# Kernel tuning notes

Measured on AMD Instinct MI355X. Metric: run time of the kernel, lower is better.

## Reference

```python
import jax, jax.numpy as jnp
import numpy as np

L, B, H = 4096, 32, 512


def setup_inputs() -> dict:
    key = jax.random.key(0)
    k1, k2, k3, k4 = jax.random.split(key, 4)
    query = jax.random.normal(k1, (B, H), dtype=jnp.float32)
    key_val = jax.random.normal(k2, (L, B, H), dtype=jnp.float32)
    # torch Linear(2H, H, bias=False): weight is (H, 2H); we store transposed (2H, H)
    W = jax.random.normal(k3, (2 * H, H), dtype=jnp.float32) * (1.0 / np.sqrt(2 * H))
    v = jax.random.normal(k4, (H,), dtype=jnp.float32)
    return {"query": query, "key_val": key_val, "W": W, "v": v}


def reference(query, key_val, W, v):
    # concat([expand(query), key], -1) @ W == query @ W_q + key @ W_k
    Wq, Wk = W[:H], W[H:]                       # each (H, H)
    q_proj = query @ Wq                          # (B, H)
    k_proj = jnp.einsum('lbi,ih->lbh', key_val, Wk)  # (L, B, H)
    energy = jnp.tanh(q_proj[None, :, :] + k_proj)   # (L, B, H)
    scores = jnp.einsum('h,lbh->bl', v, energy)      # (B, L)
    return jax.nn.softmax(scores, axis=1)[:, None, :]  # (B, 1, L)
```

## Files before the change

kernel.cpp:

```cpp
#include <hip/hip_runtime.h>
#include <hip/hip_bf16.h>
#include <stdint.h>

#define L_DIM 4096
#define B_DIM 32
#define H_DIM 512
#define M_DIM (L_DIM * B_DIM)
#define K_DIM H_DIM

typedef _Float16 half8 __attribute__((ext_vector_type(8)));
typedef __fp16 fp16x2 __attribute__((ext_vector_type(2)));
typedef float floatx4 __attribute__((ext_vector_type(4)));

__device__ __forceinline__ float tanh_fast(float x) {
  float e = __builtin_amdgcn_exp2f(x * 2.88539008177793f);
  return 1.0f - 2.0f * __builtin_amdgcn_rcpf(e + 1.0f);
}

__device__ __forceinline__ uint2 pack4(const float4& f) {
  const fp16x2 p0 = __builtin_amdgcn_cvt_pkrtz(f.x, f.y);
  const fp16x2 p1 = __builtin_amdgcn_cvt_pkrtz(f.z, f.w);
  uint2 u;
  u.x = __builtin_bit_cast(unsigned, p0);
  u.y = __builtin_bit_cast(unsigned, p1);
  return u;
}

__global__ __launch_bounds__(128) void qproj_kernel(const float* __restrict__ query,
                                                    const float* __restrict__ W,
                                                    float* __restrict__ qp) {
  const int b = blockIdx.x;
  const int h = threadIdx.x * 4;
  const float* qrow = query + b * H_DIM;
  float4 acc = make_float4(0.f, 0.f, 0.f, 0.f);
#pragma unroll 8
  for (int i = 0; i < K_DIM; ++i) {
    const float qv = qrow[i];
    const float4 w4 = *(const float4*)(W + (size_t)i * H_DIM + h);
    acc.x += qv * w4.x; acc.y += qv * w4.y;
    acc.z += qv * w4.z; acc.w += qv * w4.w;
  }
  *(float4*)(qp + (size_t)b * H_DIM + h) = acc;
}

__global__ __launch_bounds__(256) void wconv_kernel(const float* __restrict__ W,
                                                    _Float16* __restrict__ W2) {
  const int t = blockIdx.x * 256 + threadIdx.x;
  const int l15 = t & 15;
  const int q = (t >> 4) & 3;
  const int nc = (t >> 6) & 31;
  const int kt = t >> 11;
  const int n = nc * 16 + l15;
  const int kbase = H_DIM + kt * 32 + q * 8;
  half8 h;
#pragma unroll
  for (int j = 0; j < 8; ++j)
    h[j] = (_Float16)W[(size_t)(kbase + j) * H_DIM + n];
  *(half8*)(W2 + (size_t)t * 8) = h;
}

__global__ __launch_bounds__(256, 2) void fused_gemm_kernel(
    const float* __restrict__ key, const _Float16* __restrict__ W2,
    const float* __restrict__ qp, const float* __restrict__ v,
    float* __restrict__ scores) {
  __shared__ __align__(16) _Float16 As[2][64 * 40];
  __shared__ float swave[256];

  const int tid = threadIdx.x;
  const int lane = tid & 63;
  const int w = tid >> 6;
  const int l15 = lane & 15;
  const int quad = lane >> 4;
  const int m0 = blockIdx.x * 64;

  const int ar = tid >> 3;
  const int aseg = tid & 7;
  const float* ag0 = key + (size_t)(m0 + ar) * K_DIM + aseg * 4;
  const float* ag1 = ag0 + (size_t)32 * K_DIM;
  const int adst0 = ar * 40 + aseg * 4;
  const int adst1 = (ar + 32) * 40 + aseg * 4;

  const half8* bptr = (const half8*)W2 + (size_t)(w * 8) * 64 + lane;

  int aoff[4];
#pragma unroll
  for (int fm = 0; fm < 4; ++fm) aoff[fm] = (fm * 16 + l15) * 40 + quad * 8;

  floatx4 acc[4][8];
#pragma unroll
  for (int fm = 0; fm < 4; ++fm)
#pragma unroll
    for (int fn = 0; fn < 8; ++fn) acc[fm][fn] = (floatx4)0.0f;

  float4 ra0 = *(const float4*)(ag0);
  float4 ra1 = *(const float4*)(ag1);
  half8 bn[8];
#pragma unroll
  for (int fn = 0; fn < 8; ++fn) bn[fn] = bptr[fn * 64];
  bptr += 32 * 64;
  *(uint2*)(As[0] + adst0) = pack4(ra0);
  *(uint2*)(As[0] + adst1) = pack4(ra1);
  ra0 = *(const float4*)(ag0 + 32);
  ra1 = *(const float4*)(ag1 + 32);
  __syncthreads();

  for (int kt = 0; kt < 16; ++kt) {
    half8 bc[8];
#pragma unroll
    for (int fn = 0; fn < 8; ++fn) bc[fn] = bn[fn];
    if (kt < 15) {
#pragma unroll
      for (int fn = 0; fn < 8; ++fn) bn[fn] = bptr[fn * 64];
      bptr += 32 * 64;
    }
    half8 av[4];
#pragma unroll
    for (int fm = 0; fm < 4; ++fm) av[fm] = *(const half8*)(As[kt & 1] + aoff[fm]);
    if (kt < 15) {
      _Float16* dst = As[(kt + 1) & 1];
      *(uint2*)(dst + adst0) = pack4(ra0);
      *(uint2*)(dst + adst1) = pack4(ra1);
      if (kt < 14) {
        ra0 = *(const float4*)(ag0 + (kt + 2) * 32);
        ra1 = *(const float4*)(ag1 + (kt + 2) * 32);
      }
    }
#pragma unroll
    for (int fm = 0; fm < 4; ++fm)
#pragma unroll
      for (int fn = 0; fn < 8; ++fn)
        acc[fm][fn] = __builtin_amdgcn_mfma_f32_16x16x32_f16(av[fm], bc[fn],
                                                             acc[fm][fn], 0, 0, 0);
    __syncthreads();
  }

  float vv[8];
#pragma unroll
  for (int fn = 0; fn < 8; ++fn) vv[fn] = v[w * 128 + fn * 16 + l15];

#pragma unroll
  for (int fm = 0; fm < 4; ++fm) {
#pragma unroll
    for (int r = 0; r < 4; ++r) {
      const int mrow = fm * 16 + quad * 4 + r;
      const float* qrow = qp + (size_t)(mrow & 31) * H_DIM;
      float rs = 0.f;
#pragma unroll
      for (int fn = 0; fn < 8; ++fn) {
        const int n = w * 128 + fn * 16 + l15;
        const float x = qrow[n] + acc[fm][fn][r];
        rs += vv[fn] * tanh_fast(x);
      }
      rs += __shfl_xor(rs, 1);
      rs += __shfl_xor(rs, 2);
      rs += __shfl_xor(rs, 4);
      rs += __shfl_xor(rs, 8);
      if (l15 == 0) swave[w * 64 + mrow] = rs;
    }
  }
  __syncthreads();
  if (tid < 64) {
    const float s = swave[tid] + swave[64 + tid] + swave[128 + tid] + swave[192 + tid];
    const int m = m0 + tid;
    scores[(size_t)(m & 31) * L_DIM + (m >> 5)] = s;
  }
}

__global__ __launch_bounds__(256) void softmax_kernel(const float* __restrict__ scores,
                                                      float* __restrict__ out) {
  const int b = blockIdx.x;
  const int t = threadIdx.x;
  __shared__ float red[256];
  const float* srow = scores + (size_t)b * L_DIM;
  float s[16];
#pragma unroll
  for (int i = 0; i < 16; ++i) s[i] = srow[t + i * 256];
  float mx = s[0];
#pragma unroll
  for (int i = 1; i < 16; ++i) mx = fmaxf(mx, s[i]);
  red[t] = mx;
  __syncthreads();
  for (int off = 128; off > 0; off >>= 1) {
    if (t < off) red[t] = fmaxf(red[t], red[t + off]);
    __syncthreads();
  }
  mx = red[0];
  __syncthreads();
  float sum = 0.f;
#pragma unroll
  for (int i = 0; i < 16; ++i) {
    s[i] = __builtin_amdgcn_exp2f((s[i] - mx) * 1.44269504f);
    sum += s[i];
  }
  red[t] = sum;
  __syncthreads();
  for (int off = 128; off > 0; off >>= 1) {
    if (t < off) red[t] += red[t + off];
    __syncthreads();
  }
  const float inv = 1.0f / red[0];
#pragma unroll
  for (int i = 0; i < 16; ++i) out[(size_t)b * L_DIM + t + i * 256] = s[i] * inv;
}

extern "C" void kernel_launch(void* const* d_in, const int* in_sizes, int n_in,
                              void* d_out, int out_size, void* d_ws, size_t ws_size,
                              hipStream_t stream) {
  const float* query = (const float*)d_in[0];
  const float* key   = (const float*)d_in[1];
  const float* W     = (const float*)d_in[2];
  const float* v     = (const float*)d_in[3];
  float* out = (float*)d_out;

  char* ws = (char*)d_ws;
  float* qp       = (float*)ws;
  float* scores   = (float*)(ws + 65536);
  _Float16* W2    = (_Float16*)(ws + 65536 + 524288);

  qproj_kernel<<<32, 128, 0, stream>>>(query, W, qp);
  wconv_kernel<<<128, 256, 0, stream>>>(W, W2);
  fused_gemm_kernel<<<M_DIM / 64, 256, 0, stream>>>(key, W2, qp, v, scores);
  softmax_kernel<<<B_DIM, 256, 0, stream>>>(scores, out);
}
```

Before: 446.8 us.

## Stage full A tile in swizzled LDS and drop per-k-step barriers

Loads the entire 64x512 key tile for a block into LDS as fp16 up front, using an XOR swizzle to avoid bank conflicts. The K loop then runs without any __syncthreads, prefetching the next A fragments from LDS into registers. This removes the per-iteration barriers and the double-buffer store traffic. In exchange LDS use grows to 64 KB per block, which can limit occupancy, and all global loads are issued before any compute, so load/compute overlap within a block is lost.

Result: slower. 485.7 us (+8.7%).

```diff
diff --git a/kernel.cpp b/kernel.cpp
--- a/kernel.cpp
+++ b/kernel.cpp
@@ -63,8 +63,7 @@
     const float* __restrict__ key, const _Float16* __restrict__ W2,
     const float* __restrict__ qp, const float* __restrict__ v,
     float* __restrict__ scores) {
-  __shared__ __align__(16) _Float16 As[2][64 * 40];
-  __shared__ float swave[256];
+  __shared__ __align__(16) _Float16 As[64 * 512];
 
   const int tid = threadIdx.x;
   const int lane = tid & 63;
@@ -73,18 +72,24 @@
   const int quad = lane >> 4;
   const int m0 = blockIdx.x * 64;
 
-  const int ar = tid >> 3;
-  const int aseg = tid & 7;
-  const float* ag0 = key + (size_t)(m0 + ar) * K_DIM + aseg * 4;
-  const float* ag1 = ag0 + (size_t)32 * K_DIM;
-  const int adst0 = ar * 40 + aseg * 4;
-  const int adst1 = (ar + 32) * 40 + aseg * 4;
+  {
+    const float* gsrc = key + (size_t)m0 * K_DIM;
+#pragma unroll
+    for (int i = 0; i < 32; ++i) {
+      const int c = i * 256 + tid;
+      const float4 f = *(const float4*)(gsrc + 4 * c);
+      const int row = c >> 7;
+      const int off = row * 1024 + ((((c & 127) >> 1) ^ (row & 7)) << 4) + (c & 1) * 8;
+      *(uint2*)((char*)As + off) = pack4(f);
+    }
+  }
 
   const half8* bptr = (const half8*)W2 + (size_t)(w * 8) * 64 + lane;
 
-  int aoff[4];
-#pragma unroll
-  for (int fm = 0; fm < 4; ++fm) aoff[fm] = (fm * 16 + l15) * 40 + quad * 8;
+  int abase[4];
+#pragma unroll
+  for (int fm = 0; fm < 4; ++fm) abase[fm] = (fm * 16 + l15) * 1024;
+  const int xorv = l15 & 7;
 
   floatx4 acc[4][8];
 #pragma unroll
@@ -92,38 +97,34 @@
 #pragma unroll
     for (int fn = 0; fn < 8; ++fn) acc[fm][fn] = (floatx4)0.0f;
 
-  float4 ra0 = *(const float4*)(ag0);
-  float4 ra1 = *(const float4*)(ag1);
   half8 bn[8];
 #pragma unroll
   for (int fn = 0; fn < 8; ++fn) bn[fn] = bptr[fn * 64];
   bptr += 32 * 64;
-  *(uint2*)(As[0] + adst0) = pack4(ra0);
-  *(uint2*)(As[0] + adst1) = pack4(ra1);
-  ra0 = *(const float4*)(ag0 + 32);
-  ra1 = *(const float4*)(ag1 + 32);
-  __syncthreads();
+
+  __syncthreads();
+
+  half8 av[4];
+  {
+    const int coff = ((0 * 4 + quad) ^ xorv) << 4;
+#pragma unroll
+    for (int fm = 0; fm < 4; ++fm)
+      av[fm] = *(const half8*)((const char*)As + abase[fm] + coff);
+  }
 
   for (int kt = 0; kt < 16; ++kt) {
     half8 bc[8];
 #pragma unroll
     for (int fn = 0; fn < 8; ++fn) bc[fn] = bn[fn];
+    half8 an[4];
     if (kt < 15) {
 #pragma unroll
       for (int fn = 0; fn < 8; ++fn) bn[fn] = bptr[fn * 64];
       bptr += 32 * 64;
-    }
-    half8 av[4];
-#pragma unroll
-    for (int fm = 0; fm < 4; ++fm) av[fm] = *(const half8*)(As[kt & 1] + aoff[fm]);
-    if (kt < 15) {
-      _Float16* dst = As[(kt + 1) & 1];
-      *(uint2*)(dst + adst0) = pack4(ra0);
-      *(uint2*)(dst + adst1) = pack4(ra1);
-      if (kt < 14) {
-        ra0 = *(const float4*)(ag0 + (kt + 2) * 32);
-        ra1 = *(const float4*)(ag1 + (kt + 2) * 32);
-      }
+      const int coff = (((kt + 1) * 4 + quad) ^ xorv) << 4;
+#pragma unroll
+      for (int fm = 0; fm < 4; ++fm)
+        an[fm] = *(const half8*)((const char*)As + abase[fm] + coff);
     }
 #pragma unroll
     for (int fm = 0; fm < 4; ++fm)
@@ -131,13 +132,17 @@
       for (int fn = 0; fn < 8; ++fn)
         acc[fm][fn] = __builtin_amdgcn_mfma_f32_16x16x32_f16(av[fm], bc[fn],
                                                              acc[fm][fn], 0, 0, 0);
-    __syncthreads();
+    if (kt < 15) {
+#pragma unroll
+      for (int fm = 0; fm < 4; ++fm) av[fm] = an[fm];
+    }
   }
 
   float vv[8];
 #pragma unroll
   for (int fn = 0; fn < 8; ++fn) vv[fn] = v[w * 128 + fn * 16 + l15];
 
+  float rsav[4][4];
 #pragma unroll
   for (int fm = 0; fm < 4; ++fm) {
 #pragma unroll
@@ -155,9 +160,17 @@
       rs += __shfl_xor(rs, 2);
       rs += __shfl_xor(rs, 4);
       rs += __shfl_xor(rs, 8);
-      if (l15 == 0) swave[w * 64 + mrow] = rs;
-    }
-  }
+      rsav[fm][r] = rs;
+    }
+  }
+
+  __syncthreads();
+  float* swave = (float*)As;
+#pragma unroll
+  for (int fm = 0; fm < 4; ++fm)
+#pragma unroll
+    for (int r = 0; r < 4; ++r)
+      if (l15 == 0) swave[w * 64 + fm * 16 + quad * 4 + r] = rsav[fm][r];
   __syncthreads();
   if (tid < 64) {
     const float s = swave[tid] + swave[64 + tid] + swave[128 + tid] + swave[192 + tid];
```
